# Kernel optimization log

Hardware: AMD Instinct MI355X
Metric: run time of the kernel (lower is better)

Reference implementation:

```python
import jax, jax.numpy as jnp
import numpy as np

KH, KW = 3, 3
STRIDE = 1
PADDING = 1
CIN, COUT = 64, 64


def setup_inputs() -> dict:
    key = jax.random.key(0)
    kx, kw, kb = jax.random.split(key, 3)
    x = jax.random.normal(kx, (16, CIN, 112, 112), dtype=jnp.float32)
    # Kaiming-uniform style init, matching the torch module
    fan = CIN * KH * KW
    gain = np.sqrt(2.0)
    bound_w = np.sqrt(3.0) * gain / np.sqrt(fan)
    weights = jax.random.uniform(kw, (COUT, CIN, KH, KW), dtype=jnp.float32,
                                 minval=-bound_w, maxval=bound_w)
    bound_b = 1.0 / np.sqrt(fan)
    bias = jax.random.uniform(kb, (COUT,), dtype=jnp.float32,
                              minval=-bound_b, maxval=bound_b)
    return {"x": x, "weights": weights, "bias": bias}


def reference(x, weights, bias):
    # Equivalent to F.unfold + GEMM: a standard cross-correlation conv.
    # x: (N, C, H, W), weights: (F, C, KH, KW) -> out: (N, F, H', W')
    out = jax.lax.conv_general_dilated(
        x, weights,
        window_strides=(STRIDE, STRIDE),
        padding=((PADDING, PADDING), (PADDING, PADDING)),
        dimension_numbers=("NCHW", "OIHW", "NCHW"),
    )
    return out + bias[None, :, None, None]
```

## Files before the change

### kernel.cpp

```cpp
#include <hip/hip_runtime.h>


typedef __attribute__((ext_vector_type(8))) short bf16x8;
typedef __attribute__((ext_vector_type(4))) float f32x4;

#define CIN 64
#define COUT 64
#define HH 112
#define WW 112
#define ROWS 2
#define TILES 7
#define STRIPH (ROWS * TILES)
#define NPL 8
#define WPITCH 67
#define PLANE_SHORTS (8 * WPITCH * 8)
#define LDS_SHORTS (NPL * PLANE_SHORTS)

__device__ __forceinline__ int ladr(int pl, int oct, int w) {
    return ((pl * 8 + oct) * WPITCH + w) * 8;
}

__device__ __forceinline__ unsigned short f2bf(float f) {
    unsigned u = __builtin_bit_cast(unsigned, f);
    u += 0x7FFFu + ((u >> 16) & 1u);
    return (unsigned short)(u >> 16);
}

#if __has_builtin(__builtin_amdgcn_cvt_pk_bf16_f32)
__device__ __forceinline__ unsigned pk2bf(float a, float b) {
    typedef __attribute__((ext_vector_type(2))) __bf16 bf16x2;
    bf16x2 r = __builtin_amdgcn_cvt_pk_bf16_f32(a, b);
    return __builtin_bit_cast(unsigned, r);
}
#else
__device__ __forceinline__ unsigned pk2bf(float a, float b) {
    return (unsigned)f2bf(a) | ((unsigned)f2bf(b) << 16);
}
#endif

#define BAR_LGKM() do {                                   \
    __builtin_amdgcn_sched_barrier(0);                    \
    asm volatile("s_waitcnt lgkmcnt(0)" ::: "memory");    \
    __builtin_amdgcn_s_barrier();                         \
    __builtin_amdgcn_sched_barrier(0);                    \
} while (0)

__global__ void conv_wprep(const float* __restrict__ w, short* __restrict__ wbf) {
    int i = blockIdx.x * 256 + threadIdx.x;
    int j = i & 7;
    int f = (i >> 3) & 63;
    int koct = (i >> 9) & 3;
    int cb = (i >> 11) & 1;
    int t = i >> 12;
    int c = cb * 32 + koct * 8 + j;
    int ky = t / 3, kx = t - ky * 3;
    wbf[i] = (short)f2bf(w[((f * CIN + c) * 3 + ky) * 3 + kx]);
}

struct StageRegs {
    float4 v[8];
    float hv;
};

__device__ __forceinline__ void stage_load(const float* __restrict__ x, int tid,
                                           int n, int c0, int W4N, int gce,
                                           int row0, StageRegs& sr)
{
    if (tid < 256) {
        const int re = tid >> 7, oct = (tid >> 4) & 7, w4 = tid & 15;
        const int row = row0 + re;
#pragma unroll
        for (int k = 0; k < 8; ++k) sr.v[k] = (float4){0.f, 0.f, 0.f, 0.f};
        if ((unsigned)row < (unsigned)HH && w4 < W4N) {
            const float* px = x + (((n * CIN + oct * 8) * HH + row) * WW + c0 + w4 * 4);
#pragma unroll
            for (int k = 0; k < 8; ++k) sr.v[k] = *(const float4*)(px + k * HH * WW);
        }
    } else if (tid < 384) {
        const int i = tid - 256;
        const int row = row0 + (i >> 6);
        sr.hv = 0.f;
        if ((unsigned)row < (unsigned)HH)
            sr.hv = x[((n * CIN + (i & 63)) * HH + row) * WW + gce];
    }
}

__device__ __forceinline__ void stage_write(short* lds, int tid, int W4N,
                                            int padw, int wedge, int row0,
                                            const StageRegs& sr)
{
    if (tid < 256) {
        const int re = tid >> 7, oct = (tid >> 4) & 7, w4 = tid & 15;
        const int pl = (row0 + re) & (NPL - 1);
        if (w4 < W4N) {
            const float* fv = (const float*)&sr.v[0];
#pragma unroll
            for (int dw = 0; dw < 4; ++dw) {
                uint4 pk;
                pk.x = pk2bf(fv[0 * 4 + dw], fv[1 * 4 + dw]);
                pk.y = pk2bf(fv[2 * 4 + dw], fv[3 * 4 + dw]);
                pk.z = pk2bf(fv[4 * 4 + dw], fv[5 * 4 + dw]);
                pk.w = pk2bf(fv[6 * 4 + dw], fv[7 * 4 + dw]);
                *(uint4*)&lds[ladr(pl, oct, 1 + w4 * 4 + dw)] = pk;
            }
        }
    } else if (tid < 384) {
        const int i = tid - 256;
        const int row = row0 + (i >> 6);
        const int pl = row & (NPL - 1);
        const int c = i & 63;
        lds[ladr(pl, c >> 3, wedge) + (c & 7)] = (short)f2bf(sr.hv);
    } else if (tid < 400) {
        const int i = tid - 384;
        const int pl = (row0 + (i >> 3)) & (NPL - 1);
        *(uint4*)&lds[ladr(pl, i & 7, padw)] = (uint4){0u, 0u, 0u, 0u};
    }
}

__global__ __launch_bounds__(512, 2)
void conv3x3_mfma(const float* __restrict__ x, const short* __restrict__ wbf,
                  const float* __restrict__ bias, float* __restrict__ out)
{
    __shared__ __align__(16) short lds[LDS_SHORTS];
    const int tid = threadIdx.x;
    const int n = blockIdx.x;
    const int ws = blockIdx.y;
    const int hb = blockIdx.z * STRIPH;

    const int MTN   = ws ? 3 : 4;
    const int W4N   = ws ? 12 : 16;
    const int c0    = ws * 64;
    const int padw  = ws ? 49 : 0;
    const int gce   = ws ? 63 : 64;
    const int wedge = ws ? 0 : 65;

    const int wave = tid >> 6;
    const int r  = wave >> 2;
    const int nh = (wave >> 1) & 1;
    const int mh = wave & 1;
    const int lane = tid & 63;
    const int lm = lane & 15;
    const int q  = lane >> 4;

    StageRegs sr;

    stage_load(x, tid, n, c0, W4N, gce, hb - 1, sr);
    stage_write(lds, tid, W4N, padw, wedge, hb - 1, sr);
    stage_load(x, tid, n, c0, W4N, gce, hb + 1, sr);
    stage_write(lds, tid, W4N, padw, wedge, hb + 1, sr);

    bf16x8 bw[9][2][2];
#pragma unroll
    for (int t = 0; t < 9; ++t)
#pragma unroll
        for (int ntl = 0; ntl < 2; ++ntl) {
            const int f = nh * 32 + ntl * 16 + lm;
            bw[t][ntl][0] = *(const bf16x8*)(wbf + (t * 8 + q) * 512 + f * 8);
            bw[t][ntl][1] = *(const bf16x8*)(wbf + (t * 8 + 4 + q) * 512 + f * 8);
        }
#pragma unroll
    for (int t = 0; t < 9; ++t)
#pragma unroll
        for (int ntl = 0; ntl < 2; ++ntl)
#pragma unroll
            for (int cb = 0; cb < 2; ++cb)
                asm volatile("" : "=v"(bw[t][ntl][cb]) : "0"(bw[t][ntl][cb]));

    const int f0 = nh * 32 + lm;
    const float b0 = bias[f0];
    const float b1 = bias[f0 + 16];

    BAR_LGKM();

#pragma unroll 1
    for (int t = 0; t < TILES; ++t) {
        const int h0 = hb + 2 * t;
        const bool do_stage = (t < TILES - 1);

        if (do_stage) stage_load(x, tid, n, c0, W4N, gce, h0 + 3, sr);

        f32x4 acc[2][2];
#pragma unroll
        for (int j = 0; j < 2; ++j)
#pragma unroll
            for (int ntl = 0; ntl < 2; ++ntl) acc[j][ntl] = (f32x4){0.f, 0.f, 0.f, 0.f};

#pragma unroll
        for (int tap = 0; tap < 9; ++tap) {
            const int ky = tap / 3, kx = tap - ky * 3;
            const int pl = (h0 - 1 + r + ky) & (NPL - 1);
#pragma unroll
            for (int j = 0; j < 2; ++j) {
                const int mt = mh * 2 + j;
                if (mt < MTN) {
                    const int wcol = mt * 16 + lm + kx;
                    const bf16x8 a0 = *(const bf16x8*)&lds[ladr(pl, q, wcol)];
                    const bf16x8 a1 = *(const bf16x8*)&lds[ladr(pl, q + 4, wcol)];
                    acc[j][0] = __builtin_amdgcn_mfma_f32_16x16x32_bf16(a0, bw[tap][0][0], acc[j][0], 0, 0, 0);
                    acc[j][1] = __builtin_amdgcn_mfma_f32_16x16x32_bf16(a0, bw[tap][1][0], acc[j][1], 0, 0, 0);
                    acc[j][0] = __builtin_amdgcn_mfma_f32_16x16x32_bf16(a1, bw[tap][0][1], acc[j][0], 0, 0, 0);
                    acc[j][1] = __builtin_amdgcn_mfma_f32_16x16x32_bf16(a1, bw[tap][1][1], acc[j][1], 0, 0, 0);
                }
            }
        }

        if (do_stage) stage_write(lds, tid, W4N, padw, wedge, h0 + 3, sr);

        const int hrow = h0 + r;
#pragma unroll
        for (int j = 0; j < 2; ++j) {
            const int mt = mh * 2 + j;
            if (mt < MTN) {
#pragma unroll
                for (int ntl = 0; ntl < 2; ++ntl) {
                    const f32x4 v = acc[j][ntl];
                    const float bb = ntl ? b1 : b0;
                    float4 s;
                    s.x = v[0] + bb; s.y = v[1] + bb; s.z = v[2] + bb; s.w = v[3] + bb;
                    *(float4*)(out + ((n * COUT + f0 + ntl * 16) * HH + hrow) * WW
                               + c0 + mt * 16 + q * 4) = s;
                }
            }
        }

        BAR_LGKM();
    }
}

extern "C" void kernel_launch(void* const* d_in, const int* in_sizes, int n_in,
                              void* d_out, int out_size, void* d_ws, size_t ws_size,
                              hipStream_t stream) {
    const float* x = (const float*)d_in[0];
    const float* w = (const float*)d_in[1];
    const float* b = (const float*)d_in[2];
    float* out = (float*)d_out;
    short* wbf = (short*)d_ws;

    conv_wprep<<<144, 256, 0, stream>>>(w, wbf);
    dim3 grid(16, 2, 8);
    conv3x3_mfma<<<grid, 512, 0, stream>>>(x, wbf, b, out);
}
```

Baseline: 116.2 us.

## Stream conv weights from global memory instead of pinning them in registers

Stops holding all 36 bf16x8 weight fragments in VGPRs for the whole kernel and instead reloads them from the global workspace inside the tile loop for every m-tile. The tap and m-tile loops are reordered so that all 18 LDS activation fragments for an m-tile are loaded up front before the MFMAs run. The aim is to lower register pressure under the 512-thread, 2-block launch bounds and batch the LDS reads. The cost is a large amount of repeated global/L2 weight traffic on the MFMA critical path, and each m-tile's weights are fetched again per tile.

Result: slower. 177.4 us (+52.6%).

```diff
diff --git a/kernel.cpp b/kernel.cpp
--- a/kernel.cpp
+++ b/kernel.cpp
@@ -149,26 +149,10 @@
     stage_load(x, tid, n, c0, W4N, gce, hb + 1, sr);
     stage_write(lds, tid, W4N, padw, wedge, hb + 1, sr);
 
-    bf16x8 bw[9][2][2];
-#pragma unroll
-    for (int t = 0; t < 9; ++t)
-#pragma unroll
-        for (int ntl = 0; ntl < 2; ++ntl) {
-            const int f = nh * 32 + ntl * 16 + lm;
-            bw[t][ntl][0] = *(const bf16x8*)(wbf + (t * 8 + q) * 512 + f * 8);
-            bw[t][ntl][1] = *(const bf16x8*)(wbf + (t * 8 + 4 + q) * 512 + f * 8);
-        }
-#pragma unroll
-    for (int t = 0; t < 9; ++t)
-#pragma unroll
-        for (int ntl = 0; ntl < 2; ++ntl)
-#pragma unroll
-            for (int cb = 0; cb < 2; ++cb)
-                asm volatile("" : "=v"(bw[t][ntl][cb]) : "0"(bw[t][ntl][cb]));
-
     const int f0 = nh * 32 + lm;
     const float b0 = bias[f0];
     const float b1 = bias[f0 + 16];
+    const short* wb_base = wbf + q * 512 + f0 * 8;
 
     BAR_LGKM();
 
@@ -186,20 +170,29 @@
             for (int ntl = 0; ntl < 2; ++ntl) acc[j][ntl] = (f32x4){0.f, 0.f, 0.f, 0.f};
 
 #pragma unroll
-        for (int tap = 0; tap < 9; ++tap) {
-            const int ky = tap / 3, kx = tap - ky * 3;
-            const int pl = (h0 - 1 + r + ky) & (NPL - 1);
-#pragma unroll
-            for (int j = 0; j < 2; ++j) {
-                const int mt = mh * 2 + j;
-                if (mt < MTN) {
+        for (int j = 0; j < 2; ++j) {
+            const int mt = mh * 2 + j;
+            if (mt < MTN) {
+                bf16x8 af[9][2];
+#pragma unroll
+                for (int tap = 0; tap < 9; ++tap) {
+                    const int ky = tap / 3, kx = tap - ky * 3;
+                    const int pl = (h0 - 1 + r + ky) & (NPL - 1);
                     const int wcol = mt * 16 + lm + kx;
-                    const bf16x8 a0 = *(const bf16x8*)&lds[ladr(pl, q, wcol)];
-                    const bf16x8 a1 = *(const bf16x8*)&lds[ladr(pl, q + 4, wcol)];
-                    acc[j][0] = __builtin_amdgcn_mfma_f32_16x16x32_bf16(a0, bw[tap][0][0], acc[j][0], 0, 0, 0);
-                    acc[j][1] = __builtin_amdgcn_mfma_f32_16x16x32_bf16(a0, bw[tap][1][0], acc[j][1], 0, 0, 0);
-                    acc[j][0] = __builtin_amdgcn_mfma_f32_16x16x32_bf16(a1, bw[tap][0][1], acc[j][0], 0, 0, 0);
-                    acc[j][1] = __builtin_amdgcn_mfma_f32_16x16x32_bf16(a1, bw[tap][1][1], acc[j][1], 0, 0, 0);
+                    af[tap][0] = *(const bf16x8*)&lds[ladr(pl, q, wcol)];
+                    af[tap][1] = *(const bf16x8*)&lds[ladr(pl, q + 4, wcol)];
+                }
+#pragma unroll
+                for (int tap = 0; tap < 9; ++tap) {
+                    const short* wb = wb_base + tap * 8 * 512;
+                    const bf16x8 b00 = *(const bf16x8*)(wb);
+                    const bf16x8 b01 = *(const bf16x8*)(wb + 128);
+                    const bf16x8 b10 = *(const bf16x8*)(wb + 4 * 512);
+                    const bf16x8 b11 = *(const bf16x8*)(wb + 4 * 512 + 128);
+                    acc[j][0] = __builtin_amdgcn_mfma_f32_16x16x32_bf16(af[tap][0], b00, acc[j][0], 0, 0, 0);
+                    acc[j][1] = __builtin_amdgcn_mfma_f32_16x16x32_bf16(af[tap][0], b01, acc[j][1], 0, 0, 0);
+                    acc[j][0] = __builtin_amdgcn_mfma_f32_16x16x32_bf16(af[tap][1], b10, acc[j][0], 0, 0, 0);
+                    acc[j][1] = __builtin_amdgcn_mfma_f32_16x16x32_bf16(af[tap][1], b11, acc[j][1], 0, 0, 0);
                 }
             }
         }
```
